# Kernel optimization log

Measured on AMD Instinct MI355X. Metric: run time of the kernel, lower is better.

The kernel has to match this reference:

```python
import jax, jax.numpy as jnp
import numpy as np

FEATURE_DIM = 256
KEEP = 64  # low-frequency block size kept after the pseudo-DCT


def setup_inputs() -> dict:
    key = jax.random.key(0)
    k_x, k_w, k_b = jax.random.split(key, 3)
    B, C, H, W = 32, 3, 512, 512
    x = jax.random.uniform(k_x, (B, C, H, W), dtype=jnp.float32)
    # nn.Linear(64*64, feature_dim): weight [out, in], bias [out]
    fan_in = KEEP * KEEP
    bound = 1.0 / np.sqrt(fan_in)
    fc_w = jax.random.uniform(k_w, (FEATURE_DIM, fan_in), dtype=jnp.float32, minval=-bound, maxval=bound)
    fc_b = jax.random.uniform(k_b, (FEATURE_DIM,), dtype=jnp.float32, minval=-bound, maxval=bound)
    return {"x": x, "fc_w": fc_w, "fc_b": fc_b}


def reference(x, fc_w, fc_b):
    # grayscale conversion (input has 3 channels)
    x_gray = 0.299 * x[:, 0] + 0.587 * x[:, 1] + 0.114 * x[:, 2]  # [B, H, W]
    # "dct2d": FFT along last dim, then FFT along second-to-last, real part
    X = jnp.fft.fft(jnp.fft.fft(x_gray, axis=-1), axis=-2).real  # [B, H, W]
    # keep low-frequency 64x64 block and flatten
    coeffs = X[:, :KEEP, :KEEP].reshape(x.shape[0], KEEP * KEEP)  # [B, 4096]
    # final linear projection
    return coeffs @ fc_w.T + fc_b  # [B, feature_dim]
```

## Files before the change

kernel.cpp:

```cpp
#include <hip/hip_runtime.h>

#define HW_ (512 * 512)

typedef __attribute__((ext_vector_type(8))) _Float16 half8;
typedef __attribute__((ext_vector_type(4))) _Float16 half4;
typedef __attribute__((ext_vector_type(4))) float    f32x4;

__global__ __launch_bounds__(256) void k_prep(const float* __restrict__ fc_w,
                                              _Float16* __restrict__ bF1,
                                              _Float16* __restrict__ bF2,
                                              _Float16* __restrict__ whF)
{
    int id = blockIdx.x * 256 + threadIdx.x;
    if (id < 65536) {
        int j = id & 7, lane = (id >> 3) & 63;
        int mt = (id >> 9) & 7, ks = id >> 12;
        int m = mt * 16 + (lane & 15);
        int k = ks * 32 + ((lane >> 4) << 3) + j;
        int ph = ((m & 63) * k) & 511;
        float ang = (float)ph * (6.28318530717958647692f / 512.0f);
        bF1[id] = (_Float16)((m < 64) ? cosf(ang) : sinf(ang));
    } else if (id < 131072) {
        int id2 = id - 65536;
        int j = id2 & 7, lane = (id2 >> 3) & 63;
        int kt = (id2 >> 9) & 3, t = id2 >> 11;
        int kh = kt * 16 + (lane & 15);
        int kg = t * 32 + ((lane >> 4) << 3) + j;
        int h = kg & 511;
        int ph = (kh * h) & 511;
        float ang = (float)ph * (6.28318530717958647692f / 512.0f);
        bF2[id2] = (_Float16)((kg < 512) ? cosf(ang) : sinf(ang));
    } else {
        int idx8 = id - 131072;
        int lane = idx8 & 63;
        int f = ((idx8 >> 6) & 15) * 16 + (lane & 15);
        int k = (idx8 >> 10) * 32 + ((lane >> 4) << 3);
        const float* wp = fc_w + (size_t)f * 4096 + k;
        float4 f0 = *(const float4*)wp;
        float4 f1 = *(const float4*)(wp + 4);
        half8 o;
        o[0] = (_Float16)(f0.x * 16.0f);
        o[1] = (_Float16)(f0.y * 16.0f);
        o[2] = (_Float16)(f0.z * 16.0f);
        o[3] = (_Float16)(f0.w * 16.0f);
        o[4] = (_Float16)(f1.x * 16.0f);
        o[5] = (_Float16)(f1.y * 16.0f);
        o[6] = (_Float16)(f1.z * 16.0f);
        o[7] = (_Float16)(f1.w * 16.0f);
        *(half8*)(whF + (size_t)idx8 * 8) = o;
    }
}

__global__ __launch_bounds__(256) void k1(const float* __restrict__ x,
                                          const _Float16* __restrict__ bF1,
                                          _Float16* __restrict__ PF)
{
    __shared__ _Float16 g[16][520];
    int h0 = blockIdx.x * 16;
    int b  = blockIdx.y;
    int t  = threadIdx.x;
    const float* xb = x + (size_t)b * 3 * HW_;

    for (int i = 0; i < 8; ++i) {
        int slot = t + i * 256;
        int hh = slot >> 7, w4 = slot & 127;
        const float* p = xb + (size_t)(h0 + hh) * 512 + w4 * 4;
        float4 r  = *(const float4*)p;
        float4 gg = *(const float4*)(p + HW_);
        float4 bb = *(const float4*)(p + 2 * HW_);
        half4 o;
        o.x = (_Float16)(0.299f * r.x + 0.587f * gg.x + 0.114f * bb.x);
        o.y = (_Float16)(0.299f * r.y + 0.587f * gg.y + 0.114f * bb.y);
        o.z = (_Float16)(0.299f * r.z + 0.587f * gg.z + 0.114f * bb.z);
        o.w = (_Float16)(0.299f * r.w + 0.587f * gg.w + 0.114f * bb.w);
        *(half4*)&g[hh][w4 * 4] = o;
    }
    __syncthreads();

    int lane = t & 63, wv = t >> 6, l15 = lane & 15, quad = lane >> 4;
    f32x4 acc[2];
    acc[0] = (f32x4){0.f, 0.f, 0.f, 0.f};
    acc[1] = (f32x4){0.f, 0.f, 0.f, 0.f};

    for (int k0 = 0; k0 < 512; k0 += 32) {
        half8 bv = *(const half8*)&g[l15][k0 + quad * 8];
        for (int mi = 0; mi < 2; ++mi) {
            half8 a = *(const half8*)(bF1 +
                (size_t)(((k0 >> 5) * 8 + wv * 2 + mi) * 64 + lane) * 8);
            acc[mi] = __builtin_amdgcn_mfma_f32_16x16x32_f16(a, bv, acc[mi], 0, 0, 0);
        }
    }

    _Float16* Pb = PF + (size_t)b * 65536;
    int h = h0 + l15;
    for (int mi = 0; mi < 2; ++mi)
        for (int r = 0; r < 4; ++r) {
            int m = wv * 32 + mi * 16 + quad * 4 + r;
            float v = acc[mi][r];
            int m64 = m & 63;
            int tt  = (m < 64) ? (h >> 5) : 16 + (h >> 5);
            if (m >= 64) v = -v;
            int lp = (m64 & 15) | (((h >> 3) & 3) << 4);
            Pb[(size_t)((tt * 4 + (m64 >> 4)) * 64 + lp) * 8 + (h & 7)] = (_Float16)v;
        }
}

__global__ __launch_bounds__(256) void k2(const _Float16* __restrict__ bF2,
                                          const _Float16* __restrict__ PF,
                                          _Float16* __restrict__ XF)
{
    __shared__ float red[2][64][17];
    int b = blockIdx.y;
    int lane = threadIdx.x & 63, wv = threadIdx.x >> 6;
    int l15 = lane & 15, quad = lane >> 4;
    int khtile = blockIdx.x * 2 + (wv & 1);
    int khalf  = wv >> 1;

    const _Float16* Pb = PF + (size_t)b * 65536;
    f32x4 acc[4];
    for (int i = 0; i < 4; ++i) acc[i] = (f32x4){0.f, 0.f, 0.f, 0.f};

    int t0 = khalf * 16;
    for (int tt = t0; tt < t0 + 16; ++tt) {
        half8 a = *(const half8*)(bF2 + (size_t)((tt * 4 + khtile) * 64 + lane) * 8);
        for (int ni = 0; ni < 4; ++ni) {
            half8 bv = *(const half8*)(Pb + (size_t)((tt * 4 + ni) * 64 + lane) * 8);
            acc[ni] = __builtin_amdgcn_mfma_f32_16x16x32_f16(a, bv, acc[ni], 0, 0, 0);
        }
    }

    if (khalf)
        for (int ni = 0; ni < 4; ++ni)
            for (int r = 0; r < 4; ++r)
                red[wv & 1][lane][ni * 4 + r] = acc[ni][r];
    __syncthreads();
    if (!khalf)
        for (int ni = 0; ni < 4; ++ni)
            for (int r = 0; r < 4; ++r) {
                float v = acc[ni][r] + red[wv][lane][ni * 4 + r];
                int kh = khtile * 16 + quad * 4 + r;
                int kw = ni * 16 + l15;
                int k  = kh * 64 + kw;
                int lp = (b & 15) | (((k >> 3) & 3) << 4);
                XF[(size_t)(((k >> 5) * 2 + (b >> 4)) * 64 + lp) * 8 + (k & 7)] =
                    (_Float16)(v * 0.0625f);
            }
}

__global__ __launch_bounds__(512) void k3(const _Float16* __restrict__ XF,
                                          const _Float16* __restrict__ whF,
                                          const float* __restrict__ fc_b,
                                          float* __restrict__ out)
{
    __shared__ float red[8][64][9];
    int nb = blockIdx.x;
    int tid = threadIdx.x;
    int lane = tid & 63, wv = tid >> 6;

    f32x4 acc[2];
    acc[0] = (f32x4){0.f, 0.f, 0.f, 0.f};
    acc[1] = (f32x4){0.f, 0.f, 0.f, 0.f};

    for (int it = 0; it < 16; ++it) {
        int tt = wv * 16 + it;
        half8 a0 = *(const half8*)(XF + (size_t)((tt * 2 + 0) * 64 + lane) * 8);
        half8 a1 = *(const half8*)(XF + (size_t)((tt * 2 + 1) * 64 + lane) * 8);
        half8 bv = *(const half8*)(whF + (size_t)((tt * 16 + nb) * 64 + lane) * 8);
        acc[0] = __builtin_amdgcn_mfma_f32_16x16x32_f16(a0, bv, acc[0], 0, 0, 0);
        acc[1] = __builtin_amdgcn_mfma_f32_16x16x32_f16(a1, bv, acc[1], 0, 0, 0);
    }

    for (int j = 0; j < 8; ++j)
        red[wv][lane][j] = acc[j >> 2][j & 3];
    __syncthreads();

    int lp = tid >> 3, j = tid & 7;
    float s = 0.f;
    for (int w = 0; w < 8; ++w) s += red[w][lp][j];
    int batch = (j >> 2) * 16 + (lp >> 4) * 4 + (j & 3);
    int f = nb * 16 + (lp & 15);
    out[batch * 256 + f] = s + fc_b[f];
}

extern "C" void kernel_launch(void* const* d_in, const int* in_sizes, int n_in,
                              void* d_out, int out_size, void* d_ws, size_t ws_size,
                              hipStream_t stream) {
    const float* x    = (const float*)d_in[0];
    const float* fc_w = (const float*)d_in[1];
    const float* fc_b = (const float*)d_in[2];
    float* out = (float*)d_out;

    char* ws = (char*)d_ws;
    _Float16* bF1 = (_Float16*)(ws);
    _Float16* bF2 = (_Float16*)(ws + 131072);
    _Float16* whF = (_Float16*)(ws + 262144);
    _Float16* PF  = (_Float16*)(ws + 2359296);
    _Float16* XF  = (_Float16*)(ws + 6553600);

    k_prep<<<1024, 256, 0, stream>>>(fc_w, bF1, bF2, whF);
    k1<<<dim3(32, 32), 256, 0, stream>>>(x, bF1, PF);
    k2<<<dim3(2, 32), 256, 0, stream>>>(bF2, PF, XF);
    k3<<<16, 512, 0, stream>>>(XF, whF, fc_b, out);
}
```

Baseline: 178.4 us.

## Generate twiddles inline and fold weight conversion into first kernel

Removes the separate prep kernel. DFT twiddle factors are now computed on the fly with fast __sinf/__cosf inside the MFMA loops, and the fc weight fp16 conversion runs in an extra column of blocks in k1. k2 is split four ways along the reduction dimension with four blocks per batch instead of two, which adds parallelism and a 3-way LDS reduction. The cost is extra transcendental ALU work per MFMA, plus slightly lower accuracy from the fast sin/cos intrinsics.

Measured after the change: 171.2 us. 4.0% less time.

```diff
diff --git a/kernel.cpp b/kernel.cpp
--- a/kernel.cpp
+++ b/kernel.cpp
@@ -1,64 +1,68 @@
 #include <hip/hip_runtime.h>
 
 #define HW_ (512 * 512)
+#define TWOPI_512 0.01227184630308513f
 
 typedef __attribute__((ext_vector_type(8))) _Float16 half8;
 typedef __attribute__((ext_vector_type(4))) _Float16 half4;
 typedef __attribute__((ext_vector_type(4))) float    f32x4;
 
-__global__ __launch_bounds__(256) void k_prep(const float* __restrict__ fc_w,
-                                              _Float16* __restrict__ bF1,
-                                              _Float16* __restrict__ bF2,
-                                              _Float16* __restrict__ whF)
-{
-    int id = blockIdx.x * 256 + threadIdx.x;
-    if (id < 65536) {
-        int j = id & 7, lane = (id >> 3) & 63;
-        int mt = (id >> 9) & 7, ks = id >> 12;
-        int m = mt * 16 + (lane & 15);
-        int k = ks * 32 + ((lane >> 4) << 3) + j;
-        int ph = ((m & 63) * k) & 511;
-        float ang = (float)ph * (6.28318530717958647692f / 512.0f);
-        bF1[id] = (_Float16)((m < 64) ? cosf(ang) : sinf(ang));
-    } else if (id < 131072) {
-        int id2 = id - 65536;
-        int j = id2 & 7, lane = (id2 >> 3) & 63;
-        int kt = (id2 >> 9) & 3, t = id2 >> 11;
-        int kh = kt * 16 + (lane & 15);
-        int kg = t * 32 + ((lane >> 4) << 3) + j;
-        int h = kg & 511;
-        int ph = (kh * h) & 511;
-        float ang = (float)ph * (6.28318530717958647692f / 512.0f);
-        bF2[id2] = (_Float16)((kg < 512) ? cosf(ang) : sinf(ang));
-    } else {
-        int idx8 = id - 131072;
-        int lane = idx8 & 63;
-        int f = ((idx8 >> 6) & 15) * 16 + (lane & 15);
-        int k = (idx8 >> 10) * 32 + ((lane >> 4) << 3);
-        const float* wp = fc_w + (size_t)f * 4096 + k;
-        float4 f0 = *(const float4*)wp;
-        float4 f1 = *(const float4*)(wp + 4);
-        half8 o;
-        o[0] = (_Float16)(f0.x * 16.0f);
-        o[1] = (_Float16)(f0.y * 16.0f);
-        o[2] = (_Float16)(f0.z * 16.0f);
-        o[3] = (_Float16)(f0.w * 16.0f);
-        o[4] = (_Float16)(f1.x * 16.0f);
-        o[5] = (_Float16)(f1.y * 16.0f);
-        o[6] = (_Float16)(f1.z * 16.0f);
-        o[7] = (_Float16)(f1.w * 16.0f);
-        *(half8*)(whF + (size_t)idx8 * 8) = o;
+template<bool SIN>
+__device__ __forceinline__ void k1_loop(const _Float16 (*g)[520],
+                                        int l15, int quad, int mk0, int mk1,
+                                        f32x4& acc0, f32x4& acc1)
+{
+    for (int k0 = 0; k0 < 512; k0 += 32) {
+        int kc = k0 + quad * 8;
+        half8 bv = *(const half8*)&g[l15][kc];
+        half8 a0, a1;
+#pragma unroll
+        for (int j = 0; j < 8; ++j) {
+            int k = kc + j;
+            float ang0 = (float)(__mul24(mk0, k) & 511) * TWOPI_512;
+            float ang1 = (float)(__mul24(mk1, k) & 511) * TWOPI_512;
+            a0[j] = (_Float16)(SIN ? __sinf(ang0) : __cosf(ang0));
+            a1[j] = (_Float16)(SIN ? __sinf(ang1) : __cosf(ang1));
+        }
+        acc0 = __builtin_amdgcn_mfma_f32_16x16x32_f16(a0, bv, acc0, 0, 0, 0);
+        acc1 = __builtin_amdgcn_mfma_f32_16x16x32_f16(a1, bv, acc1, 0, 0, 0);
     }
 }
 
 __global__ __launch_bounds__(256) void k1(const float* __restrict__ x,
-                                          const _Float16* __restrict__ bF1,
-                                          _Float16* __restrict__ PF)
+                                          const float* __restrict__ fc_w,
+                                          _Float16* __restrict__ PF,
+                                          _Float16* __restrict__ whF)
 {
     __shared__ _Float16 g[16][520];
+    int t = threadIdx.x;
+
+    if (blockIdx.x == 32) {
+        int pid = blockIdx.y;
+        for (int it = 0; it < 16; ++it) {
+            int idx8 = pid * 4096 + it * 256 + t;
+            int lane = idx8 & 63;
+            int f = ((idx8 >> 6) & 15) * 16 + (lane & 15);
+            int k = (idx8 >> 10) * 32 + ((lane >> 4) << 3);
+            const float* wp = fc_w + (size_t)f * 4096 + k;
+            float4 f0 = *(const float4*)wp;
+            float4 f1 = *(const float4*)(wp + 4);
+            half8 o;
+            o[0] = (_Float16)(f0.x * 16.0f);
+            o[1] = (_Float16)(f0.y * 16.0f);
+            o[2] = (_Float16)(f0.z * 16.0f);
+            o[3] = (_Float16)(f0.w * 16.0f);
+            o[4] = (_Float16)(f1.x * 16.0f);
+            o[5] = (_Float16)(f1.y * 16.0f);
+            o[6] = (_Float16)(f1.z * 16.0f);
+            o[7] = (_Float16)(f1.w * 16.0f);
+            *(half8*)(whF + (size_t)idx8 * 8) = o;
+        }
+        return;
+    }
+
     int h0 = blockIdx.x * 16;
     int b  = blockIdx.y;
-    int t  = threadIdx.x;
     const float* xb = x + (size_t)b * 3 * HW_;
 
     for (int i = 0; i < 8; ++i) {
@@ -78,18 +82,15 @@
     __syncthreads();
 
     int lane = t & 63, wv = t >> 6, l15 = lane & 15, quad = lane >> 4;
+    int mk0 = (wv * 32 + l15) & 63;
+    int mk1 = (wv * 32 + 16 + l15) & 63;
+
     f32x4 acc[2];
     acc[0] = (f32x4){0.f, 0.f, 0.f, 0.f};
     acc[1] = (f32x4){0.f, 0.f, 0.f, 0.f};
 
-    for (int k0 = 0; k0 < 512; k0 += 32) {
-        half8 bv = *(const half8*)&g[l15][k0 + quad * 8];
-        for (int mi = 0; mi < 2; ++mi) {
-            half8 a = *(const half8*)(bF1 +
-                (size_t)(((k0 >> 5) * 8 + wv * 2 + mi) * 64 + lane) * 8);
-            acc[mi] = __builtin_amdgcn_mfma_f32_16x16x32_f16(a, bv, acc[mi], 0, 0, 0);
-        }
-    }
+    if (wv >= 2) k1_loop<true >(g, l15, quad, mk0, mk1, acc[0], acc[1]);
+    else         k1_loop<false>(g, l15, quad, mk0, mk1, acc[0], acc[1]);
 
     _Float16* Pb = PF + (size_t)b * 65536;
     int h = h0 + l15;
@@ -105,43 +106,60 @@
         }
 }
 
-__global__ __launch_bounds__(256) void k2(const _Float16* __restrict__ bF2,
-                                          const _Float16* __restrict__ PF,
+template<bool SIN>
+__device__ __forceinline__ void k2_loop(const _Float16* __restrict__ Pb,
+                                        int t0, int kh, int quad, int lane,
+                                        f32x4* acc)
+{
+    for (int it = 0; it < 8; ++it) {
+        int tt = t0 + it;
+        int kgb = tt * 32 + quad * 8;
+        half8 a;
+#pragma unroll
+        for (int j = 0; j < 8; ++j) {
+            int h = (kgb + j) & 511;
+            float ang = (float)(__mul24(kh, h) & 511) * TWOPI_512;
+            a[j] = (_Float16)(SIN ? __sinf(ang) : __cosf(ang));
+        }
+        for (int ni = 0; ni < 4; ++ni) {
+            half8 bv = *(const half8*)(Pb + (size_t)((tt * 4 + ni) * 64 + lane) * 8);
+            acc[ni] = __builtin_amdgcn_mfma_f32_16x16x32_f16(a, bv, acc[ni], 0, 0, 0);
+        }
+    }
+}
+
+__global__ __launch_bounds__(256) void k2(const _Float16* __restrict__ PF,
                                           _Float16* __restrict__ XF)
 {
-    __shared__ float red[2][64][17];
-    int b = blockIdx.y;
+    __shared__ float red[3][64][17];
+    int b  = blockIdx.y;
+    int bx = blockIdx.x;
     int lane = threadIdx.x & 63, wv = threadIdx.x >> 6;
     int l15 = lane & 15, quad = lane >> 4;
-    int khtile = blockIdx.x * 2 + (wv & 1);
-    int khalf  = wv >> 1;
+    int kh = bx * 16 + l15;
 
     const _Float16* Pb = PF + (size_t)b * 65536;
     f32x4 acc[4];
     for (int i = 0; i < 4; ++i) acc[i] = (f32x4){0.f, 0.f, 0.f, 0.f};
 
-    int t0 = khalf * 16;
-    for (int tt = t0; tt < t0 + 16; ++tt) {
-        half8 a = *(const half8*)(bF2 + (size_t)((tt * 4 + khtile) * 64 + lane) * 8);
-        for (int ni = 0; ni < 4; ++ni) {
-            half8 bv = *(const half8*)(Pb + (size_t)((tt * 4 + ni) * 64 + lane) * 8);
-            acc[ni] = __builtin_amdgcn_mfma_f32_16x16x32_f16(a, bv, acc[ni], 0, 0, 0);
-        }
-    }
-
-    if (khalf)
+    if (wv >= 2) k2_loop<true >(Pb, wv * 8, kh, quad, lane, acc);
+    else         k2_loop<false>(Pb, wv * 8, kh, quad, lane, acc);
+
+    if (wv)
         for (int ni = 0; ni < 4; ++ni)
             for (int r = 0; r < 4; ++r)
-                red[wv & 1][lane][ni * 4 + r] = acc[ni][r];
+                red[wv - 1][lane][ni * 4 + r] = acc[ni][r];
     __syncthreads();
-    if (!khalf)
+    if (!wv)
         for (int ni = 0; ni < 4; ++ni)
             for (int r = 0; r < 4; ++r) {
-                float v = acc[ni][r] + red[wv][lane][ni * 4 + r];
-                int kh = khtile * 16 + quad * 4 + r;
-                int kw = ni * 16 + l15;
-                int k  = kh * 64 + kw;
-                int lp = (b & 15) | (((k >> 3) & 3) << 4);
+                float v = acc[ni][r] + red[0][lane][ni * 4 + r]
+                                     + red[1][lane][ni * 4 + r]
+                                     + red[2][lane][ni * 4 + r];
+                int khr = bx * 16 + quad * 4 + r;
+                int kw  = ni * 16 + l15;
+                int k   = khr * 64 + kw;
+                int lp  = (b & 15) | (((k >> 3) & 3) << 4);
                 XF[(size_t)(((k >> 5) * 2 + (b >> 4)) * 64 + lp) * 8 + (k & 7)] =
                     (_Float16)(v * 0.0625f);
             }
@@ -191,14 +209,11 @@
     float* out = (float*)d_out;
 
     char* ws = (char*)d_ws;
-    _Float16* bF1 = (_Float16*)(ws);
-    _Float16* bF2 = (_Float16*)(ws + 131072);
-    _Float16* whF = (_Float16*)(ws + 262144);
-    _Float16* PF  = (_Float16*)(ws + 2359296);
-    _Float16* XF  = (_Float16*)(ws + 6553600);
-
-    k_prep<<<1024, 256, 0, stream>>>(fc_w, bF1, bF2, whF);
-    k1<<<dim3(32, 32), 256, 0, stream>>>(x, bF1, PF);
-    k2<<<dim3(2, 32), 256, 0, stream>>>(bF2, PF, XF);
+    _Float16* PF  = (_Float16*)(ws);
+    _Float16* XF  = (_Float16*)(ws + 4194304);
+    _Float16* whF = (_Float16*)(ws + 4456448);
+
+    k1<<<dim3(33, 32), 256, 0, stream>>>(x, fc_w, PF, whF);
+    k2<<<dim3(4, 32),  256, 0, stream>>>(PF, XF);
     k3<<<16, 512, 0, stream>>>(XF, whF, fc_b, out);
 }
```
